# Performance work log

Measured on AMD Instinct MI355X. Metric: run time of the kernel, lower is better.

Reference implementation:

```python
import jax, jax.numpy as jnp
import numpy as np

N_NODES = 50000
N_EDGES = 800000
N_GRAPHS = 512
IN_CH, HID_CH, OUT_CH, N_CLASSES = 128, 64, 64, 10


def gcn_conv(x, src, dst, ew, W, b, n_nodes):
    """PyG GCNConv: add self-loops (weight 1), symmetric normalization, x @ W, scatter-add at dst, + bias."""
    xw = x @ W  # [N, out]
    loop = jnp.arange(n_nodes, dtype=src.dtype)
    src_f = jnp.concatenate([src, loop])
    dst_f = jnp.concatenate([dst, loop])
    ew_f = jnp.concatenate([ew, jnp.ones((n_nodes,), dtype=ew.dtype)])
    deg = jax.ops.segment_sum(ew_f, dst_f, num_segments=n_nodes)  # [N]
    dinv = jnp.where(deg > 0, jax.lax.rsqrt(deg), 0.0)
    norm = dinv[src_f] * ew_f * dinv[dst_f]  # [E+N]
    msg = norm[:, None] * xw[src_f]  # gather + scale
    out = jax.ops.segment_sum(msg, dst_f, num_segments=n_nodes)  # scatter-add
    return out + b


def setup_inputs() -> dict:
    key = jax.random.key(0)
    ks = jax.random.split(key, 12)
    x = jax.random.normal(ks[0], (N_NODES, IN_CH), dtype=jnp.float32)
    edge_index = jax.random.randint(ks[1], (2, N_EDGES), 0, N_NODES, dtype=jnp.int64)
    edge_attr = jax.random.uniform(ks[2], (N_EDGES,), dtype=jnp.float32)
    batch = jnp.sort(jax.random.randint(ks[3], (N_NODES,), 0, N_GRAPHS, dtype=jnp.int64))
    def glorot(k, shape):
        lim = np.sqrt(6.0 / (shape[0] + shape[1]))
        return jax.random.uniform(k, shape, jnp.float32, -lim, lim)
    W1 = glorot(ks[4], (IN_CH, HID_CH))
    b1 = jnp.zeros((HID_CH,), jnp.float32)
    W2 = glorot(ks[5], (HID_CH, OUT_CH))
    b2 = jnp.zeros((OUT_CH,), jnp.float32)
    LW1 = glorot(ks[6], (OUT_CH, 32))
    Lb1 = jnp.zeros((32,), jnp.float32)
    LW2 = glorot(ks[7], (32, N_CLASSES))
    Lb2 = jnp.zeros((N_CLASSES,), jnp.float32)
    return {"x": x, "edge_index": edge_index, "edge_attr": edge_attr, "batch": batch,
            "W1": W1, "b1": b1, "W2": W2, "b2": b2,
            "LW1": LW1, "Lb1": Lb1, "LW2": LW2, "Lb2": Lb2}


def reference(x, edge_index, edge_attr, batch, W1, b1, W2, b2, LW1, Lb1, LW2, Lb2):
    src, dst = edge_index[0], edge_index[1]
    h = gcn_conv(x, src, dst, edge_attr, W1, b1, N_NODES)
    h = jax.nn.relu(h)
    h = gcn_conv(h, src, dst, edge_attr, W2, b2, N_NODES)
    # global mean pool over graphs
    sums = jax.ops.segment_sum(h, batch, num_segments=N_GRAPHS)  # [G, OUT]
    cnt = jax.ops.segment_sum(jnp.ones((N_NODES,), h.dtype), batch, num_segments=N_GRAPHS)
    pooled = sums / jnp.maximum(cnt, 1.0)[:, None]
    # head (dropout treated as identity for deterministic reference)
    h1 = pooled @ LW1 + Lb1
    return h1 @ LW2 + Lb2
```

## Files before the change

kernel.cpp:

```cpp
#include <hip/hip_runtime.h>
#include <hip/hip_bf16.h>

static constexpr int NN = 50000;
static constexpr int NE = 800000;
static constexpr int NG = 512;
static constexpr int NB = 196;
static constexpr int NTILES = (NN + 63) / 64;
static constexpr int KSLOT = 64;

__device__ __forceinline__ float bfu(ushort u) {
    return __uint_as_float((unsigned)u << 16);
}
__device__ __forceinline__ ushort fbf(float f) {
    return __hip_bfloat16_raw(__float2bfloat16(f)).x;
}
__device__ __forceinline__ void bf8_unpack(uint4 u, float* f) {
    f[0] = __uint_as_float(u.x << 16); f[1] = __uint_as_float(u.x & 0xffff0000u);
    f[2] = __uint_as_float(u.y << 16); f[3] = __uint_as_float(u.y & 0xffff0000u);
    f[4] = __uint_as_float(u.z << 16); f[5] = __uint_as_float(u.z & 0xffff0000u);
    f[6] = __uint_as_float(u.w << 16); f[7] = __uint_as_float(u.w & 0xffff0000u);
}

__global__ void zero_kernel(float* __restrict__ p, int n) {
    int i = blockIdx.x * blockDim.x + threadIdx.x;
    if (i < n) p[i] = 0.f;
}

__global__ void hist_ell_kernel(const int* __restrict__ src, const int* __restrict__ dst,
                                const float* __restrict__ ew, unsigned* __restrict__ h,
                                int2* __restrict__ epack) {
    int e = blockIdx.x * blockDim.x + threadIdx.x;
    if (e >= NE) return;
    int d = dst[e];
    float w = ew[e];
    unsigned fx = __float2uint_rn(w * 1024.0f);
    unsigned old = atomicAdd(&h[d], (1u << 24) | fx);
    int rank = (int)(old >> 24);
    epack[d * KSLOT + rank] = make_int2(src[e], __float_as_int(w));
}

__global__ __launch_bounds__(256) void dinv_bounds_kernel(const unsigned* __restrict__ h,
                                                          float* __restrict__ dinv,
                                                          const int* __restrict__ batch,
                                                          int* __restrict__ gbeg,
                                                          int* __restrict__ gend) {
    int i = blockIdx.x * 256 + threadIdx.x;
    if (i >= NN) return;
    float deg = (float)(h[i] & 0xFFFFFFu) * (1.0f / 1024.0f) + 1.0f;
    dinv[i] = 1.0f / sqrtf(deg);
    int g = batch[i];
    if (i == 0 || batch[i - 1] != g) gbeg[g] = i;
    if (i == NN - 1 || batch[i + 1] != g) gend[g] = i + 1;
}

__global__ __launch_bounds__(256) void gemm128_kernel(const float* __restrict__ X,
                                                      const float* __restrict__ W1,
                                                      ushort* __restrict__ out) {
    __shared__ float Xs[64][68];
    __shared__ ushort Wsb[128 * 64];
    int t = threadIdx.x;
    int row0 = blockIdx.x * 64;
    for (int i = t; i < 128 * 16; i += 256) {
        float4 w = ((const float4*)W1)[i];
        ushort4 s; s.x = fbf(w.x); s.y = fbf(w.y); s.z = fbf(w.z); s.w = fbf(w.w);
        *(ushort4*)&Wsb[i * 4] = s;
    }
    int tx = t & 15, ty = t >> 4;
    float acc[4][4] = {};
    for (int kb = 0; kb < 128; kb += 64) {
        __syncthreads();
        for (int i = t; i < 1024; i += 256) {
            int r = i >> 4, k4 = i & 15;
            int gr = row0 + r; if (gr >= NN) gr = NN - 1;
            *(float4*)&Xs[r][k4 * 4] = *(const float4*)(X + (long long)gr * 128 + kb + k4 * 4);
        }
        __syncthreads();
#pragma unroll
        for (int k4 = 0; k4 < 16; ++k4) {
            float4 x0 = *(const float4*)&Xs[ty * 4 + 0][k4 * 4];
            float4 x1 = *(const float4*)&Xs[ty * 4 + 1][k4 * 4];
            float4 x2 = *(const float4*)&Xs[ty * 4 + 2][k4 * 4];
            float4 x3 = *(const float4*)&Xs[ty * 4 + 3][k4 * 4];
#pragma unroll
            for (int kk = 0; kk < 4; ++kk) {
                uint2 wu = *(const uint2*)&Wsb[(kb + k4 * 4 + kk) * 64 + tx * 4];
                float w0 = __uint_as_float(wu.x << 16);
                float w1 = __uint_as_float(wu.x & 0xffff0000u);
                float w2 = __uint_as_float(wu.y << 16);
                float w3 = __uint_as_float(wu.y & 0xffff0000u);
                float xa = (&x0.x)[kk], xb = (&x1.x)[kk], xc = (&x2.x)[kk], xd = (&x3.x)[kk];
                acc[0][0] = fmaf(xa, w0, acc[0][0]); acc[0][1] = fmaf(xa, w1, acc[0][1]);
                acc[0][2] = fmaf(xa, w2, acc[0][2]); acc[0][3] = fmaf(xa, w3, acc[0][3]);
                acc[1][0] = fmaf(xb, w0, acc[1][0]); acc[1][1] = fmaf(xb, w1, acc[1][1]);
                acc[1][2] = fmaf(xb, w2, acc[1][2]); acc[1][3] = fmaf(xb, w3, acc[1][3]);
                acc[2][0] = fmaf(xc, w0, acc[2][0]); acc[2][1] = fmaf(xc, w1, acc[2][1]);
                acc[2][2] = fmaf(xc, w2, acc[2][2]); acc[2][3] = fmaf(xc, w3, acc[2][3]);
                acc[3][0] = fmaf(xd, w0, acc[3][0]); acc[3][1] = fmaf(xd, w1, acc[3][1]);
                acc[3][2] = fmaf(xd, w2, acc[3][2]); acc[3][3] = fmaf(xd, w3, acc[3][3]);
            }
        }
    }
#pragma unroll
    for (int j = 0; j < 4; ++j) {
        int r = row0 + ty * 4 + j;
        if (r < NN) {
            ushort4 sv;
            sv.x = fbf(acc[j][0]); sv.y = fbf(acc[j][1]);
            sv.z = fbf(acc[j][2]); sv.w = fbf(acc[j][3]);
            *(ushort4*)(out + (long long)r * 64 + tx * 4) = sv;
        }
    }
}

template <bool RELU>
__global__ __launch_bounds__(256) void agg_kernel(const ushort* __restrict__ xw,
                                                  const unsigned* __restrict__ h,
                                                  const int2* __restrict__ epack,
                                                  const float* __restrict__ dinv,
                                                  const float* __restrict__ bias,
                                                  ushort* __restrict__ out) {
    int node = blockIdx.x * 4 + (threadIdx.x >> 6);
    if (node >= NN) return;
    int lane = threadIdx.x & 63;
    int slot = lane >> 3;
    int l = lane & 7;
    int beg = node * KSLOT;
    int end = beg + (int)(h[node] >> 24);
    float a[8] = {}, b[8] = {};
    int j = beg + slot;
    for (; j + 8 < end; j += 16) {
        int2 pA = epack[j];
        int2 pB = epack[j + 8];
        float dA = dinv[pA.x];
        float dB = dinv[pB.x];
        uint4 uA = *(const uint4*)(xw + pA.x * 64 + 8 * l);
        uint4 uB = *(const uint4*)(xw + pB.x * 64 + 8 * l);
        float wA = dA * __int_as_float(pA.y);
        float wB = dB * __int_as_float(pB.y);
        float fA[8], fB[8];
        bf8_unpack(uA, fA);
        bf8_unpack(uB, fB);
#pragma unroll
        for (int c = 0; c < 8; ++c) {
            a[c] = fmaf(wA, fA[c], a[c]);
            b[c] = fmaf(wB, fB[c], b[c]);
        }
    }
    if (j < end) {
        int2 pA = epack[j];
        float dA = dinv[pA.x];
        uint4 uA = *(const uint4*)(xw + pA.x * 64 + 8 * l);
        float wA = dA * __int_as_float(pA.y);
        float fA[8];
        bf8_unpack(uA, fA);
#pragma unroll
        for (int c = 0; c < 8; ++c) a[c] = fmaf(wA, fA[c], a[c]);
    }
#pragma unroll
    for (int c = 0; c < 8; ++c) {
        a[c] += b[c];
        a[c] += __shfl_xor(a[c], 8);
        a[c] += __shfl_xor(a[c], 16);
        a[c] += __shfl_xor(a[c], 32);
    }
    if (slot == 0) {
        float di = dinv[node];
        float d2 = di * di;
        uint4 us = *(const uint4*)(xw + node * 64 + 8 * l);
        float fs[8];
        bf8_unpack(us, fs);
        float4 bv0 = *(const float4*)(bias + 8 * l);
        float4 bv1 = *(const float4*)(bias + 8 * l + 4);
        float o[8];
        o[0] = fmaf(di, a[0], fmaf(d2, fs[0], bv0.x));
        o[1] = fmaf(di, a[1], fmaf(d2, fs[1], bv0.y));
        o[2] = fmaf(di, a[2], fmaf(d2, fs[2], bv0.z));
        o[3] = fmaf(di, a[3], fmaf(d2, fs[3], bv0.w));
        o[4] = fmaf(di, a[4], fmaf(d2, fs[4], bv1.x));
        o[5] = fmaf(di, a[5], fmaf(d2, fs[5], bv1.y));
        o[6] = fmaf(di, a[6], fmaf(d2, fs[6], bv1.z));
        o[7] = fmaf(di, a[7], fmaf(d2, fs[7], bv1.w));
        if (RELU) {
#pragma unroll
            for (int c = 0; c < 8; ++c) o[c] = fmaxf(o[c], 0.f);
        }
        uint4 pk;
        pk.x = (unsigned)fbf(o[0]) | ((unsigned)fbf(o[1]) << 16);
        pk.y = (unsigned)fbf(o[2]) | ((unsigned)fbf(o[3]) << 16);
        pk.z = (unsigned)fbf(o[4]) | ((unsigned)fbf(o[5]) << 16);
        pk.w = (unsigned)fbf(o[6]) | ((unsigned)fbf(o[7]) << 16);
        *(uint4*)(out + node * 64 + 8 * l) = pk;
    }
}

__global__ __launch_bounds__(256) void gemm64_kernel(const ushort* __restrict__ X,
                                                     const float* __restrict__ W,
                                                     ushort* __restrict__ out) {
    __shared__ float Xs[64][68];
    __shared__ float Ws[64 * 64];
    for (int i = threadIdx.x; i < 64 * 16; i += 256)
        ((float4*)Ws)[i] = ((const float4*)W)[i];
    int tx = threadIdx.x & 15, ty = threadIdx.x >> 4;
    int row0 = blockIdx.x * 64;
    float acc[4][4] = {};
    __syncthreads();
    for (int i = threadIdx.x; i < 512; i += 256) {
        int r = i >> 3, g = i & 7;
        int gr = row0 + r; if (gr >= NN) gr = NN - 1;
        uint4 v = *(const uint4*)(X + (long long)gr * 64 + g * 8);
        float f[8];
        bf8_unpack(v, f);
        *(float4*)&Xs[r][g * 8] = make_float4(f[0], f[1], f[2], f[3]);
        *(float4*)&Xs[r][g * 8 + 4] = make_float4(f[4], f[5], f[6], f[7]);
    }
    __syncthreads();
#pragma unroll
    for (int k4 = 0; k4 < 16; ++k4) {
        float4 x0 = *(const float4*)&Xs[ty * 4 + 0][k4 * 4];
        float4 x1 = *(const float4*)&Xs[ty * 4 + 1][k4 * 4];
        float4 x2 = *(const float4*)&Xs[ty * 4 + 2][k4 * 4];
        float4 x3 = *(const float4*)&Xs[ty * 4 + 3][k4 * 4];
#pragma unroll
        for (int kk = 0; kk < 4; ++kk) {
            float4 wv = *(const float4*)&Ws[(k4 * 4 + kk) * 64 + tx * 4];
            float xa = (&x0.x)[kk], xb = (&x1.x)[kk], xc = (&x2.x)[kk], xd = (&x3.x)[kk];
            acc[0][0] = fmaf(xa, wv.x, acc[0][0]); acc[0][1] = fmaf(xa, wv.y, acc[0][1]);
            acc[0][2] = fmaf(xa, wv.z, acc[0][2]); acc[0][3] = fmaf(xa, wv.w, acc[0][3]);
            acc[1][0] = fmaf(xb, wv.x, acc[1][0]); acc[1][1] = fmaf(xb, wv.y, acc[1][1]);
            acc[1][2] = fmaf(xb, wv.z, acc[1][2]); acc[1][3] = fmaf(xb, wv.w, acc[1][3]);
            acc[2][0] = fmaf(xc, wv.x, acc[2][0]); acc[2][1] = fmaf(xc, wv.y, acc[2][1]);
            acc[2][2] = fmaf(xc, wv.z, acc[2][2]); acc[2][3] = fmaf(xc, wv.w, acc[2][3]);
            acc[3][0] = fmaf(xd, wv.x, acc[3][0]); acc[3][1] = fmaf(xd, wv.y, acc[3][1]);
            acc[3][2] = fmaf(xd, wv.z, acc[3][2]); acc[3][3] = fmaf(xd, wv.w, acc[3][3]);
        }
    }
#pragma unroll
    for (int j = 0; j < 4; ++j) {
        int r = row0 + ty * 4 + j;
        if (r < NN) {
            ushort4 sv;
            sv.x = fbf(acc[j][0]); sv.y = fbf(acc[j][1]);
            sv.z = fbf(acc[j][2]); sv.w = fbf(acc[j][3]);
            *(ushort4*)(out + (long long)r * 64 + tx * 4) = sv;
        }
    }
}

__global__ __launch_bounds__(256) void poolhead_kernel(const ushort* __restrict__ h,
                                                       const int* __restrict__ gbeg,
                                                       const int* __restrict__ gend,
                                                       const float* __restrict__ LW1,
                                                       const float* __restrict__ Lb1,
                                                       const float* __restrict__ LW2,
                                                       const float* __restrict__ Lb2,
                                                       float* __restrict__ out) {
    __shared__ float pp[4][64];
    __shared__ float p[64];
    __shared__ float t1[32];
    int g = blockIdx.x, t = threadIdx.x;
    int lane = t & 63, wid = t >> 6;
    int b = gbeg[g], e = gend[g];
    float acc = 0.f;
    for (int i = b + wid; i < e; i += 4) acc += bfu(h[i * 64 + lane]);
    pp[wid][lane] = acc;
    __syncthreads();
    if (t < 64) {
        float s = pp[0][t] + pp[1][t] + pp[2][t] + pp[3][t];
        p[t] = s / fmaxf((float)(e - b), 1.0f);
    }
    __syncthreads();
    if (t < 32) {
        float a = Lb1[t];
#pragma unroll
        for (int k = 0; k < 64; ++k) a = fmaf(p[k], LW1[k * 32 + t], a);
        t1[t] = a;
    }
    __syncthreads();
    if (t < 10) {
        float a = Lb2[t];
#pragma unroll
        for (int j = 0; j < 32; ++j) a = fmaf(t1[j], LW2[j * 10 + t], a);
        out[g * 10 + t] = a;
    }
}


extern "C" void kernel_launch(void* const* d_in, const int* in_sizes, int n_in,
                              void* d_out, int out_size, void* d_ws, size_t ws_size,
                              hipStream_t stream) {
    const float* x     = (const float*)d_in[0];
    const int*   ei    = (const int*)d_in[1];
    const float* ew    = (const float*)d_in[2];
    const int*   batch = (const int*)d_in[3];
    const float* W1    = (const float*)d_in[4];
    const float* b1    = (const float*)d_in[5];
    const float* W2    = (const float*)d_in[6];
    const float* b2    = (const float*)d_in[7];
    const float* LW1   = (const float*)d_in[8];
    const float* Lb1   = (const float*)d_in[9];
    const float* LW2   = (const float*)d_in[10];
    const float* Lb2   = (const float*)d_in[11];

    const int* src = ei;
    const int* dst = ei + NE;

    float* ws = (float*)d_ws;
    unsigned* h32 = (unsigned*)ws;
    int*   gbeg   = (int*)(ws + 50048);
    int*   gend   = (int*)(ws + 50560);
    float* dinv   = ws + 51072;
    int2*  epack  = (int2*)(ws + 101120);
    ushort* xwA   = (ushort*)(ws + 6501120);
    ushort* h12   = (ushort*)(ws + 8101120);

    zero_kernel<<<(51072 + 255) / 256, 256, 0, stream>>>(ws, 51072);

    hist_ell_kernel<<<(NE + 255) / 256, 256, 0, stream>>>(src, dst, ew, h32, epack);
    gemm128_kernel<<<NTILES, 256, 0, stream>>>(x, W1, xwA);
    dinv_bounds_kernel<<<NB, 256, 0, stream>>>(h32, dinv, batch, gbeg, gend);

    agg_kernel<true><<<(NN + 3) / 4, 256, 0, stream>>>(xwA, h32, epack, dinv, b1, h12);

    gemm64_kernel<<<NTILES, 256, 0, stream>>>(h12, W2, xwA);
    agg_kernel<false><<<(NN + 3) / 4, 256, 0, stream>>>(xwA, h32, epack, dinv, b2, h12);

    poolhead_kernel<<<NG, 256, 0, stream>>>(h12, gbeg, gend, LW1, Lb1, LW2, Lb2, (float*)d_out);
}
```

Measured before the change: 267.5 us.

## Drop dinv/bounds kernel, recompute dinv inline, split aggregation over feature halves

Removes the separate dinv_bounds kernel. The aggregation kernels now compute each node's inverse sqrt degree directly from the packed histogram word, and the pooling kernel finds graph boundaries by binary search over the sorted batch array. The aggregation grid is doubled: each block handles 32 of the 64 feature columns, with 16 edge slots per node instead of 8 and one more shuffle stage in the reduction. This cuts one launch and the dinv array traffic, and spreads the gather across more waves. In exchange, every edge's row is read twice (once per half) and each edge does an extra sqrt computation.

```diff
diff --git a/kernel.cpp b/kernel.cpp
--- a/kernel.cpp
+++ b/kernel.cpp
@@ -4,7 +4,6 @@
 static constexpr int NN = 50000;
 static constexpr int NE = 800000;
 static constexpr int NG = 512;
-static constexpr int NB = 196;
 static constexpr int NTILES = (NN + 63) / 64;
 static constexpr int KSLOT = 64;
 
@@ -20,10 +19,13 @@
     f[4] = __uint_as_float(u.z << 16); f[5] = __uint_as_float(u.z & 0xffff0000u);
     f[6] = __uint_as_float(u.w << 16); f[7] = __uint_as_float(u.w & 0xffff0000u);
 }
-
-__global__ void zero_kernel(float* __restrict__ p, int n) {
+__device__ __forceinline__ float dinv_of(unsigned hv) {
+    return 1.0f / sqrtf((float)(hv & 0xFFFFFFu) * (1.0f / 1024.0f) + 1.0f);
+}
+
+__global__ void zero_kernel(unsigned* __restrict__ p, int n) {
     int i = blockIdx.x * blockDim.x + threadIdx.x;
-    if (i < n) p[i] = 0.f;
+    if (i < n) p[i] = 0u;
 }
 
 __global__ void hist_ell_kernel(const int* __restrict__ src, const int* __restrict__ dst,
@@ -37,20 +39,6 @@
     unsigned old = atomicAdd(&h[d], (1u << 24) | fx);
     int rank = (int)(old >> 24);
     epack[d * KSLOT + rank] = make_int2(src[e], __float_as_int(w));
-}
-
-__global__ __launch_bounds__(256) void dinv_bounds_kernel(const unsigned* __restrict__ h,
-                                                          float* __restrict__ dinv,
-                                                          const int* __restrict__ batch,
-                                                          int* __restrict__ gbeg,
-                                                          int* __restrict__ gend) {
-    int i = blockIdx.x * 256 + threadIdx.x;
-    if (i >= NN) return;
-    float deg = (float)(h[i] & 0xFFFFFFu) * (1.0f / 1024.0f) + 1.0f;
-    dinv[i] = 1.0f / sqrtf(deg);
-    int g = batch[i];
-    if (i == 0 || batch[i - 1] != g) gbeg[g] = i;
-    if (i == NN - 1 || batch[i + 1] != g) gend[g] = i + 1;
 }
 
 __global__ __launch_bounds__(256) void gemm128_kernel(const float* __restrict__ X,
@@ -116,27 +104,32 @@
 __global__ __launch_bounds__(256) void agg_kernel(const ushort* __restrict__ xw,
                                                   const unsigned* __restrict__ h,
                                                   const int2* __restrict__ epack,
-                                                  const float* __restrict__ dinv,
                                                   const float* __restrict__ bias,
                                                   ushort* __restrict__ out) {
-    int node = blockIdx.x * 4 + (threadIdx.x >> 6);
+    int bid = blockIdx.x;
+    int half = (bid >> 2) & 1;
+    int grp = (bid >> 3) * 4 + (bid & 3);
+    int node = grp * 4 + (threadIdx.x >> 6);
     if (node >= NN) return;
     int lane = threadIdx.x & 63;
-    int slot = lane >> 3;
-    int l = lane & 7;
-    int beg = node * KSLOT;
-    int end = beg + (int)(h[node] >> 24);
+    int slot = lane >> 2;
+    int l = lane & 3;
+    int cb = half * 32 + 8 * l;
+    unsigned hn = h[node];
+    int deg = (int)(hn >> 24);
+    float di = dinv_of(hn);
+    int beg = node * KSLOT, end = beg + deg;
     float a[8] = {}, b[8] = {};
     int j = beg + slot;
-    for (; j + 8 < end; j += 16) {
+    for (; j + 16 < end; j += 32) {
         int2 pA = epack[j];
-        int2 pB = epack[j + 8];
-        float dA = dinv[pA.x];
-        float dB = dinv[pB.x];
-        uint4 uA = *(const uint4*)(xw + pA.x * 64 + 8 * l);
-        uint4 uB = *(const uint4*)(xw + pB.x * 64 + 8 * l);
-        float wA = dA * __int_as_float(pA.y);
-        float wB = dB * __int_as_float(pB.y);
+        int2 pB = epack[j + 16];
+        unsigned hA = h[pA.x];
+        unsigned hB = h[pB.x];
+        uint4 uA = *(const uint4*)(xw + pA.x * 64 + cb);
+        uint4 uB = *(const uint4*)(xw + pB.x * 64 + cb);
+        float wA = dinv_of(hA) * __int_as_float(pA.y);
+        float wB = dinv_of(hB) * __int_as_float(pB.y);
         float fA[8], fB[8];
         bf8_unpack(uA, fA);
         bf8_unpack(uB, fB);
@@ -148,9 +141,9 @@
     }
     if (j < end) {
         int2 pA = epack[j];
-        float dA = dinv[pA.x];
-        uint4 uA = *(const uint4*)(xw + pA.x * 64 + 8 * l);
-        float wA = dA * __int_as_float(pA.y);
+        unsigned hA = h[pA.x];
+        uint4 uA = *(const uint4*)(xw + pA.x * 64 + cb);
+        float wA = dinv_of(hA) * __int_as_float(pA.y);
         float fA[8];
         bf8_unpack(uA, fA);
 #pragma unroll
@@ -159,18 +152,18 @@
 #pragma unroll
     for (int c = 0; c < 8; ++c) {
         a[c] += b[c];
+        a[c] += __shfl_xor(a[c], 4);
         a[c] += __shfl_xor(a[c], 8);
         a[c] += __shfl_xor(a[c], 16);
         a[c] += __shfl_xor(a[c], 32);
     }
     if (slot == 0) {
-        float di = dinv[node];
         float d2 = di * di;
-        uint4 us = *(const uint4*)(xw + node * 64 + 8 * l);
+        uint4 us = *(const uint4*)(xw + node * 64 + cb);
         float fs[8];
         bf8_unpack(us, fs);
-        float4 bv0 = *(const float4*)(bias + 8 * l);
-        float4 bv1 = *(const float4*)(bias + 8 * l + 4);
+        float4 bv0 = *(const float4*)(bias + cb);
+        float4 bv1 = *(const float4*)(bias + cb + 4);
         float o[8];
         o[0] = fmaf(di, a[0], fmaf(d2, fs[0], bv0.x));
         o[1] = fmaf(di, a[1], fmaf(d2, fs[1], bv0.y));
@@ -189,7 +182,7 @@
         pk.y = (unsigned)fbf(o[2]) | ((unsigned)fbf(o[3]) << 16);
         pk.z = (unsigned)fbf(o[4]) | ((unsigned)fbf(o[5]) << 16);
         pk.w = (unsigned)fbf(o[6]) | ((unsigned)fbf(o[7]) << 16);
-        *(uint4*)(out + node * 64 + 8 * l) = pk;
+        *(uint4*)(out + node * 64 + cb) = pk;
     }
 }
 
@@ -247,19 +240,29 @@
 }
 
 __global__ __launch_bounds__(256) void poolhead_kernel(const ushort* __restrict__ h,
-                                                       const int* __restrict__ gbeg,
-                                                       const int* __restrict__ gend,
+                                                       const int* __restrict__ batch,
                                                        const float* __restrict__ LW1,
                                                        const float* __restrict__ Lb1,
                                                        const float* __restrict__ LW2,
                                                        const float* __restrict__ Lb2,
                                                        float* __restrict__ out) {
+    __shared__ int bounds[2];
     __shared__ float pp[4][64];
     __shared__ float p[64];
     __shared__ float t1[32];
     int g = blockIdx.x, t = threadIdx.x;
+    if (t < 2) {
+        int target = g + t;
+        int lo = 0, hi = NN;
+        while (lo < hi) {
+            int mid = (lo + hi) >> 1;
+            if (batch[mid] < target) lo = mid + 1; else hi = mid;
+        }
+        bounds[t] = lo;
+    }
+    __syncthreads();
+    int b = bounds[0], e = bounds[1];
     int lane = t & 63, wid = t >> 6;
-    int b = gbeg[g], e = gend[g];
     float acc = 0.f;
     for (int i = b + wid; i < e; i += 4) acc += bfu(h[i * 64 + lane]);
     pp[wid][lane] = acc;
@@ -306,23 +309,19 @@
 
     float* ws = (float*)d_ws;
     unsigned* h32 = (unsigned*)ws;
-    int*   gbeg   = (int*)(ws + 50048);
-    int*   gend   = (int*)(ws + 50560);
-    float* dinv   = ws + 51072;
-    int2*  epack  = (int2*)(ws + 101120);
-    ushort* xwA   = (ushort*)(ws + 6501120);
-    ushort* h12   = (ushort*)(ws + 8101120);
-
-    zero_kernel<<<(51072 + 255) / 256, 256, 0, stream>>>(ws, 51072);
+    int2*  epack  = (int2*)(ws + 50048);
+    ushort* xwA   = (ushort*)(ws + 6450048);
+    ushort* h12   = (ushort*)(ws + 8050048);
+
+    zero_kernel<<<(50048 + 255) / 256, 256, 0, stream>>>(h32, 50048);
 
     hist_ell_kernel<<<(NE + 255) / 256, 256, 0, stream>>>(src, dst, ew, h32, epack);
     gemm128_kernel<<<NTILES, 256, 0, stream>>>(x, W1, xwA);
-    dinv_bounds_kernel<<<NB, 256, 0, stream>>>(h32, dinv, batch, gbeg, gend);
-
-    agg_kernel<true><<<(NN + 3) / 4, 256, 0, stream>>>(xwA, h32, epack, dinv, b1, h12);
+
+    agg_kernel<true><<<25000, 256, 0, stream>>>(xwA, h32, epack, b1, h12);
 
     gemm64_kernel<<<NTILES, 256, 0, stream>>>(h12, W2, xwA);
-    agg_kernel<false><<<(NN + 3) / 4, 256, 0, stream>>>(xwA, h32, epack, dinv, b2, h12);
-
-    poolhead_kernel<<<NG, 256, 0, stream>>>(h12, gbeg, gend, LW1, Lb1, LW2, Lb2, (float*)d_out);
-}
+    agg_kernel<false><<<25000, 256, 0, stream>>>(xwA, h32, epack, b2, h12);
+
+    poolhead_kernel<<<NG, 256, 0, stream>>>(h12, batch, LW1, Lb1, LW2, Lb2, (float*)d_out);
+}
```

Result: slower. 315.6 us (+18.0%).
